# Performance work log

Hardware: AMD Instinct MI355X
Metric: run time of the kernel (lower is better)

Reference implementation:

```python
import jax, jax.numpy as jnp
import numpy as np

B, D_IN, UNITS = 4096, 1024, 1024


def setup_inputs() -> dict:
    key = jax.random.key(0)
    ks = jax.random.split(key, 8)
    scale = 1.0 / np.sqrt(D_IN + UNITS)
    return {
        "inputs": jax.random.normal(ks[0], (B, D_IN), jnp.float32),
        "hidden_state": jax.random.normal(ks[1], (B, UNITS), jnp.float32),
        "cell_state": jax.random.normal(ks[2], (B, UNITS), jnp.float32),
        "W_f": jax.random.normal(ks[3], (D_IN + UNITS, UNITS), jnp.float32) * scale,
        "b_f": jnp.ones((UNITS,), jnp.float32),  # forget gate bias initialized to ones
        "W_i": jax.random.normal(ks[4], (D_IN + UNITS, UNITS), jnp.float32) * scale,
        "b_i": jnp.zeros((UNITS,), jnp.float32),
        "W_c": jax.random.normal(ks[5], (D_IN + UNITS, UNITS), jnp.float32) * scale,
        "b_c": jnp.zeros((UNITS,), jnp.float32),
        "W_o": jax.random.normal(ks[6], (D_IN + UNITS, UNITS), jnp.float32) * scale,
        "b_o": jnp.zeros((UNITS,), jnp.float32),
    }


def reference(inputs, hidden_state, cell_state, W_f, b_f, W_i, b_i, W_c, b_c, W_o, b_o):
    # concat (hidden, inputs) along feature axis -> [B, UNITS + D_IN]
    x = jnp.concatenate((hidden_state, inputs), axis=1)
    # fuse the 4 gate projections into one GEMM: [B, 4*UNITS]
    W = jnp.concatenate((W_f, W_i, W_c, W_o), axis=1)
    b = jnp.concatenate((b_f, b_i, b_c, b_o), axis=0)
    gates = x @ W + b
    f, i, c, o = jnp.split(gates, 4, axis=1)
    forget_gate = jax.nn.sigmoid(f)
    input_gate = jax.nn.sigmoid(i)
    state_candidates = jnp.tanh(c)
    output_gate = jax.nn.sigmoid(o)
    new_cell = forget_gate * cell_state + input_gate * state_candidates
    new_hidden = output_gate * jnp.tanh(new_cell)
    return (new_hidden, new_cell)
```

## Files before the change

### kernel.cpp

```cpp
#include <hip/hip_runtime.h>

#define MDIM 4096
#define KDIM 2048
#define UDIM 1024
#define CMOFF (MDIM * UDIM)
#define NK 64
#define THREADS 512

typedef __bf16 bfrag __attribute__((ext_vector_type(8)));
typedef float f32x4 __attribute__((ext_vector_type(4)));

#define GLDS(gsrc, ldst)                                                                  \
  __builtin_amdgcn_global_load_lds((const __attribute__((address_space(1))) void*)(gsrc), \
                                   (__attribute__((address_space(3))) void*)(ldst), 16, 0, 0)

__device__ __forceinline__ unsigned short f2bf(float x) {
  unsigned int u = __float_as_uint(x);
  unsigned int r = (u + 0x7fffu + ((u >> 16) & 1u)) >> 16;
  return (unsigned short)r;
}

__device__ __forceinline__ float fast_sigmoid(float x) { return 1.f / (1.f + __expf(-x)); }

__device__ __forceinline__ float fast_tanh(float x) {
  float ax = fabsf(x);
  float e = __expf(-2.f * ax);
  float r = (1.f - e) / (1.f + e);
  return copysignf(r, x);
}

__global__ void pack_x(const float* __restrict__ hidden, const float* __restrict__ inputs,
                       unsigned short* __restrict__ A) {
  int t = blockIdx.x * blockDim.x + threadIdx.x;
  int e = t * 4;
  int m = e >> 11;
  int c = e & 2047;
  const float* src = (c < 1024) ? (hidden + m * 1024 + c) : (inputs + m * 1024 + (c - 1024));
  float4 v = *(const float4*)src;
  ushort4 o;
  o.x = f2bf(v.x);
  o.y = f2bf(v.y);
  o.z = f2bf(v.z);
  o.w = f2bf(v.w);
  *(ushort4*)(A + e) = o;
}

__global__ void pack_w(const float* __restrict__ Wf, const float* __restrict__ Wi,
                       const float* __restrict__ Wc, const float* __restrict__ Wo,
                       unsigned short* __restrict__ Wt) {
  __shared__ float tile[32][33];
  const int k0 = blockIdx.x * 32;
  const int u0 = blockIdx.y * 32;
  const int g = blockIdx.z;
  const float* W = (g == 0) ? Wf : (g == 1) ? Wi : (g == 2) ? Wc : Wo;
  const int t = threadIdx.x;
  {
    int kk = t >> 3, uu = (t & 7) * 4;
    float4 v = *(const float4*)(W + (k0 + kk) * UDIM + u0 + uu);
    tile[kk][uu + 0] = v.x;
    tile[kk][uu + 1] = v.y;
    tile[kk][uu + 2] = v.z;
    tile[kk][uu + 3] = v.w;
  }
  __syncthreads();
  {
    int ur = t >> 3, k4 = (t & 7) * 4;
    ushort4 o;
    o.x = f2bf(tile[k4 + 0][ur]);
    o.y = f2bf(tile[k4 + 1][ur]);
    o.z = f2bf(tile[k4 + 2][ur]);
    o.w = f2bf(tile[k4 + 3][ur]);
    *(ushort4*)(Wt + (size_t)(g * UDIM + u0 + ur) * KDIM + k0 + k4) = o;
  }
}

__global__ __launch_bounds__(THREADS, 2) void lstm_gemm(
    const unsigned short* __restrict__ A, const unsigned short* __restrict__ Wt,
    const float* __restrict__ bf_, const float* __restrict__ bi_,
    const float* __restrict__ bc_, const float* __restrict__ bo_,
    const float* __restrict__ cell, float* __restrict__ out) {
  extern __shared__ __bf16 lds[];

  const int tid = threadIdx.x;
  const int lane = tid & 63;
  const int wid = tid >> 6;
  const int wr = wid >> 2;
  const int wc = wid & 3;
  const int lrow = lane & 15;
  const int gb = lane >> 4;

  const int wg = blockIdx.x;
  const int swz = (wg & 7) * 32 + (wg >> 3);
  const int m0 = (swz >> 4) * 256;
  const int bn = swz & 15;

  const int G0 = tid, G1 = THREADS + tid;
  const int ar0 = G0 >> 2, ar1 = G1 >> 2;
  const unsigned short* aS0 =
      A + (size_t)(m0 + ar0) * KDIM + (((G0 & 3) ^ ((ar0 >> 1) & 3)) * 8);
  const unsigned short* aS1 =
      A + (size_t)(m0 + ar1) * KDIM + (((G1 & 3) ^ ((ar1 >> 1) & 3)) * 8);
  const int nr0 = G0 >> 2, nr1 = G1 >> 2;
  const int u_0 = bn * 64 + ((nr0 >> 6) << 4) + (nr0 & 15);
  const int u_1 = bn * 64 + ((nr1 >> 6) << 4) + (nr1 & 15);
  const int g_0 = (nr0 >> 4) & 3;
  const int g_1 = (nr1 >> 4) & 3;
  const unsigned short* bS0 =
      Wt + (size_t)(g_0 * UDIM + u_0) * KDIM + (((G0 & 3) ^ ((nr0 >> 1) & 3)) * 8);
  const unsigned short* bS1 =
      Wt + (size_t)(g_1 * UDIM + u_1) * KDIM + (((G1 & 3) ^ ((nr1 >> 1) & 3)) * 8);

  int aoff[8];
#pragma unroll
  for (int mi = 0; mi < 8; ++mi) {
    const int R = wr * 128 + mi * 16 + lrow;
    aoff[mi] = R * 32 + ((gb ^ ((R >> 1) & 3)) * 8);
  }
  int boff[4];
#pragma unroll
  for (int nf = 0; nf < 4; ++nf) {
    const int n = wc * 64 + nf * 16 + lrow;
    boff[nf] = 8192 + n * 32 + ((gb ^ ((n >> 1) & 3)) * 8);
  }

  f32x4 acc[8][4];
#pragma unroll
  for (int mi = 0; mi < 8; ++mi)
#pragma unroll
    for (int nf = 0; nf < 4; ++nf) acc[mi][nf] = (f32x4){0.f, 0.f, 0.f, 0.f};

#define STAGE_A(T, SR)                        \
  do {                                        \
    __bf16* dst_ = lds + (SR) * 16384;        \
    GLDS(aS0 + (T) * 32, dst_ + G0 * 8);      \
    GLDS(aS1 + (T) * 32, dst_ + G1 * 8);      \
  } while (0)
#define STAGE_B(T, SR)                        \
  do {                                        \
    __bf16* dst_ = lds + (SR) * 16384 + 8192; \
    GLDS(bS0 + (T) * 32, dst_ + G0 * 8);      \
    GLDS(bS1 + (T) * 32, dst_ + G1 * 8);      \
  } while (0)

  STAGE_A(0, 0);
  STAGE_B(0, 0);
  STAGE_A(1, 1);
  STAGE_B(1, 1);
  STAGE_A(2, 2);
  STAGE_B(2, 2);
  asm volatile("s_waitcnt vmcnt(8)" ::: "memory");
  __builtin_amdgcn_s_barrier();

#define TILE_BODY(T, R, SR, DO_STAGE, WAITCODE)                                        \
  do {                                                                                 \
    __bf16* ldsr_ = lds + (R) * 16384;                                                 \
    bfrag Am[4], Bm[4];                                                                \
    _Pragma("unroll") for (int mi = 0; mi < 4; ++mi) Am[mi] =                          \
        *(const bfrag*)(ldsr_ + aoff[mi]);                                             \
    _Pragma("unroll") for (int nf = 0; nf < 4; ++nf) Bm[nf] =                          \
        *(const bfrag*)(ldsr_ + boff[nf]);                                             \
    if (DO_STAGE) STAGE_A((T) + 3, SR);                                                \
    __builtin_amdgcn_s_barrier();                                                      \
    __builtin_amdgcn_s_setprio(1);                                                     \
    _Pragma("unroll") for (int mi = 0; mi < 4; ++mi)                                   \
        _Pragma("unroll") for (int nf = 0; nf < 4; ++nf) acc[mi][nf] =                 \
            __builtin_amdgcn_mfma_f32_16x16x32_bf16(Am[mi], Bm[nf], acc[mi][nf], 0, 0, 0); \
    __builtin_amdgcn_s_setprio(0);                                                     \
    bfrag A2[4];                                                                       \
    _Pragma("unroll") for (int mi = 0; mi < 4; ++mi) A2[mi] =                          \
        *(const bfrag*)(ldsr_ + aoff[4 + mi]);                                         \
    if (DO_STAGE) STAGE_B((T) + 3, SR);                                                \
    __builtin_amdgcn_s_barrier();                                                      \
    __builtin_amdgcn_s_setprio(1);                                                     \
    _Pragma("unroll") for (int mi = 0; mi < 4; ++mi)                                   \
        _Pragma("unroll") for (int nf = 0; nf < 4; ++nf) acc[4 + mi][nf] =             \
            __builtin_amdgcn_mfma_f32_16x16x32_bf16(A2[mi], Bm[nf], acc[4 + mi][nf], 0, 0, 0); \
    __builtin_amdgcn_s_setprio(0);                                                     \
    WAITCODE;                                                                          \
    __builtin_amdgcn_s_barrier();                                                      \
  } while (0)

#define VM8 asm volatile("s_waitcnt vmcnt(8)" ::: "memory")
#define VM4 asm volatile("s_waitcnt vmcnt(4)" ::: "memory")
#define VM0 asm volatile("s_waitcnt vmcnt(0)" ::: "memory")

  for (int t = 0; t < NK - 4; t += 4) {
    TILE_BODY(t + 0, 0, 3, 1, VM8);
    TILE_BODY(t + 1, 1, 0, 1, VM8);
    TILE_BODY(t + 2, 2, 1, 1, VM8);
    TILE_BODY(t + 3, 3, 2, 1, VM8);
  }
  TILE_BODY(NK - 4, 0, 3, 1, VM8);
  TILE_BODY(NK - 3, 1, 0, 0, VM4);
  TILE_BODY(NK - 2, 2, 0, 0, VM0);
  TILE_BODY(NK - 1, 3, 0, 0, );

  const int u = bn * 64 + wc * 16 + lrow;
  const float fb = bf_[u], ib = bi_[u], cb = bc_[u], ob = bo_[u];
  const int rbase = m0 + wr * 128 + (lane >> 4) * 4;
#pragma unroll
  for (int mi = 0; mi < 8; ++mi) {
#pragma unroll
    for (int j = 0; j < 4; ++j) {
      const int m = rbase + mi * 16 + j;
      float pf = acc[mi][0][j] + fb;
      float pi = acc[mi][1][j] + ib;
      float pc = acc[mi][2][j] + cb;
      float po = acc[mi][3][j] + ob;
      float fg = fast_sigmoid(pf);
      float ig = fast_sigmoid(pi);
      float cc = fast_tanh(pc);
      float og = fast_sigmoid(po);
      float cold = cell[(size_t)m * UDIM + u];
      float cnew = fg * cold + ig * cc;
      out[(size_t)m * UDIM + u] = og * fast_tanh(cnew);
      out[CMOFF + (size_t)m * UDIM + u] = cnew;
    }
  }
}

extern "C" void kernel_launch(void* const* d_in, const int* in_sizes, int n_in,
                              void* d_out, int out_size, void* d_ws, size_t ws_size,
                              hipStream_t stream) {
  const float* inputs = (const float*)d_in[0];
  const float* hidden = (const float*)d_in[1];
  const float* cell = (const float*)d_in[2];
  const float* Wf = (const float*)d_in[3];
  const float* bf = (const float*)d_in[4];
  const float* Wi = (const float*)d_in[5];
  const float* bi = (const float*)d_in[6];
  const float* Wc = (const float*)d_in[7];
  const float* bc = (const float*)d_in[8];
  const float* Wo = (const float*)d_in[9];
  const float* bo = (const float*)d_in[10];
  float* out = (float*)d_out;

  unsigned short* Abf = (unsigned short*)d_ws;
  unsigned short* Wt = Abf + (size_t)MDIM * KDIM;

  pack_x<<<(MDIM * KDIM / 4) / 256, 256, 0, stream>>>(hidden, inputs, Abf);
  pack_w<<<dim3(KDIM / 32, UDIM / 32, 4), 256, 0, stream>>>(Wf, Wi, Wc, Wo, Wt);
  lstm_gemm<<<dim3(256), dim3(THREADS), 131072, stream>>>(Abf, Wt, bf, bi, bc, bo, cell, out);
}
```

Measured before the change: 89.82 us.

## Switch GEMM to 32x32x16 MFMA with 4x2 wave layout

Replaces the 16x16x32 bf16 MFMA tiling (2x4 waves, 128x64 per wave) with 32x32x16 MFMA on a 4x2 wave grid (64x128 per wave). The B staging is permuted so each gate occupies 32-column groups, and the epilogue is remapped to the 32x32 accumulator layout. The A and B prefetches are merged into one phase with a single barrier per k-tile instead of two. The aim is fewer LDS fragment reads per MFMA and less synchronisation, at the cost of coarser overlap between loads and compute.

```diff
diff --git a/kernel.cpp b/kernel.cpp
--- a/kernel.cpp
+++ b/kernel.cpp
@@ -8,7 +8,7 @@
 #define THREADS 512
 
 typedef __bf16 bfrag __attribute__((ext_vector_type(8)));
-typedef float f32x4 __attribute__((ext_vector_type(4)));
+typedef float f32x16 __attribute__((ext_vector_type(16)));
 
 #define GLDS(gsrc, ldst)                                                                  \
   __builtin_amdgcn_global_load_lds((const __attribute__((address_space(1))) void*)(gsrc), \
@@ -84,10 +84,10 @@
   const int tid = threadIdx.x;
   const int lane = tid & 63;
   const int wid = tid >> 6;
-  const int wr = wid >> 2;
-  const int wc = wid & 3;
-  const int lrow = lane & 15;
-  const int gb = lane >> 4;
+  const int wr = wid >> 1;
+  const int wc = wid & 1;
+  const int cl = lane & 31;
+  const int hb = lane >> 5;
 
   const int wg = blockIdx.x;
   const int swz = (wg & 7) * 32 + (wg >> 3);
@@ -101,33 +101,39 @@
   const unsigned short* aS1 =
       A + (size_t)(m0 + ar1) * KDIM + (((G1 & 3) ^ ((ar1 >> 1) & 3)) * 8);
   const int nr0 = G0 >> 2, nr1 = G1 >> 2;
-  const int u_0 = bn * 64 + ((nr0 >> 6) << 4) + (nr0 & 15);
-  const int u_1 = bn * 64 + ((nr1 >> 6) << 4) + (nr1 & 15);
-  const int g_0 = (nr0 >> 4) & 3;
-  const int g_1 = (nr1 >> 4) & 3;
+  const int u_0 = bn * 64 + ((nr0 >> 7) << 5) + (nr0 & 31);
+  const int u_1 = bn * 64 + ((nr1 >> 7) << 5) + (nr1 & 31);
+  const int g_0 = (nr0 >> 5) & 3;
+  const int g_1 = (nr1 >> 5) & 3;
   const unsigned short* bS0 =
       Wt + (size_t)(g_0 * UDIM + u_0) * KDIM + (((G0 & 3) ^ ((nr0 >> 1) & 3)) * 8);
   const unsigned short* bS1 =
       Wt + (size_t)(g_1 * UDIM + u_1) * KDIM + (((G1 & 3) ^ ((nr1 >> 1) & 3)) * 8);
 
-  int aoff[8];
-#pragma unroll
-  for (int mi = 0; mi < 8; ++mi) {
-    const int R = wr * 128 + mi * 16 + lrow;
-    aoff[mi] = R * 32 + ((gb ^ ((R >> 1) & 3)) * 8);
-  }
-  int boff[4];
-#pragma unroll
-  for (int nf = 0; nf < 4; ++nf) {
-    const int n = wc * 64 + nf * 16 + lrow;
-    boff[nf] = 8192 + n * 32 + ((gb ^ ((n >> 1) & 3)) * 8);
-  }
-
-  f32x4 acc[8][4];
-#pragma unroll
-  for (int mi = 0; mi < 8; ++mi)
-#pragma unroll
-    for (int nf = 0; nf < 4; ++nf) acc[mi][nf] = (f32x4){0.f, 0.f, 0.f, 0.f};
+  int aoff2[2][2];
+#pragma unroll
+  for (int mf = 0; mf < 2; ++mf)
+#pragma unroll
+    for (int kk = 0; kk < 2; ++kk) {
+      const int R = wr * 64 + mf * 32 + cl;
+      aoff2[mf][kk] = R * 32 + (((kk * 2 + hb) ^ ((R >> 1) & 3)) * 8);
+    }
+  int boff2[4][2];
+#pragma unroll
+  for (int nf = 0; nf < 4; ++nf)
+#pragma unroll
+    for (int kk = 0; kk < 2; ++kk) {
+      const int n = wc * 128 + nf * 32 + cl;
+      boff2[nf][kk] = 8192 + n * 32 + (((kk * 2 + hb) ^ ((n >> 1) & 3)) * 8);
+    }
+
+  f32x16 acc[2][4];
+#pragma unroll
+  for (int mf = 0; mf < 2; ++mf)
+#pragma unroll
+    for (int nf = 0; nf < 4; ++nf)
+#pragma unroll
+      for (int j = 0; j < 16; ++j) acc[mf][nf][j] = 0.f;
 
 #define STAGE_A(T, SR)                        \
   do {                                        \
@@ -151,33 +157,32 @@
   asm volatile("s_waitcnt vmcnt(8)" ::: "memory");
   __builtin_amdgcn_s_barrier();
 
-#define TILE_BODY(T, R, SR, DO_STAGE, WAITCODE)                                        \
-  do {                                                                                 \
-    __bf16* ldsr_ = lds + (R) * 16384;                                                 \
-    bfrag Am[4], Bm[4];                                                                \
-    _Pragma("unroll") for (int mi = 0; mi < 4; ++mi) Am[mi] =                          \
-        *(const bfrag*)(ldsr_ + aoff[mi]);                                             \
-    _Pragma("unroll") for (int nf = 0; nf < 4; ++nf) Bm[nf] =                          \
-        *(const bfrag*)(ldsr_ + boff[nf]);                                             \
-    if (DO_STAGE) STAGE_A((T) + 3, SR);                                                \
-    __builtin_amdgcn_s_barrier();                                                      \
-    __builtin_amdgcn_s_setprio(1);                                                     \
-    _Pragma("unroll") for (int mi = 0; mi < 4; ++mi)                                   \
-        _Pragma("unroll") for (int nf = 0; nf < 4; ++nf) acc[mi][nf] =                 \
-            __builtin_amdgcn_mfma_f32_16x16x32_bf16(Am[mi], Bm[nf], acc[mi][nf], 0, 0, 0); \
-    __builtin_amdgcn_s_setprio(0);                                                     \
-    bfrag A2[4];                                                                       \
-    _Pragma("unroll") for (int mi = 0; mi < 4; ++mi) A2[mi] =                          \
-        *(const bfrag*)(ldsr_ + aoff[4 + mi]);                                         \
-    if (DO_STAGE) STAGE_B((T) + 3, SR);                                                \
-    __builtin_amdgcn_s_barrier();                                                      \
-    __builtin_amdgcn_s_setprio(1);                                                     \
-    _Pragma("unroll") for (int mi = 0; mi < 4; ++mi)                                   \
-        _Pragma("unroll") for (int nf = 0; nf < 4; ++nf) acc[4 + mi][nf] =             \
-            __builtin_amdgcn_mfma_f32_16x16x32_bf16(A2[mi], Bm[nf], acc[4 + mi][nf], 0, 0, 0); \
-    __builtin_amdgcn_s_setprio(0);                                                     \
-    WAITCODE;                                                                          \
-    __builtin_amdgcn_s_barrier();                                                      \
+#define TILE_BODY(T, R, SR, DO_STAGE, WAITCODE)                                          \
+  do {                                                                                   \
+    __bf16* ldsr_ = lds + (R) * 16384;                                                   \
+    bfrag Af[2][2], Bf[4][2];                                                            \
+    _Pragma("unroll") for (int mf = 0; mf < 2; ++mf) Af[mf][0] =                         \
+        *(const bfrag*)(ldsr_ + aoff2[mf][0]);                                           \
+    _Pragma("unroll") for (int nf = 0; nf < 4; ++nf) Bf[nf][0] =                         \
+        *(const bfrag*)(ldsr_ + boff2[nf][0]);                                           \
+    _Pragma("unroll") for (int mf = 0; mf < 2; ++mf) Af[mf][1] =                         \
+        *(const bfrag*)(ldsr_ + aoff2[mf][1]);                                           \
+    _Pragma("unroll") for (int nf = 0; nf < 4; ++nf) Bf[nf][1] =                         \
+        *(const bfrag*)(ldsr_ + boff2[nf][1]);                                           \
+    if (DO_STAGE) {                                                                      \
+      STAGE_A((T) + 3, SR);                                                              \
+      STAGE_B((T) + 3, SR);                                                              \
+    }                                                                                    \
+    __builtin_amdgcn_s_barrier();                                                        \
+    __builtin_amdgcn_s_setprio(1);                                                       \
+    _Pragma("unroll") for (int kk = 0; kk < 2; ++kk)                                     \
+        _Pragma("unroll") for (int mf = 0; mf < 2; ++mf)                                 \
+            _Pragma("unroll") for (int nf = 0; nf < 4; ++nf) acc[mf][nf] =               \
+                __builtin_amdgcn_mfma_f32_32x32x16_bf16(Af[mf][kk], Bf[nf][kk],          \
+                                                        acc[mf][nf], 0, 0, 0);           \
+    __builtin_amdgcn_s_setprio(0);                                                       \
+    WAITCODE;                                                                            \
+    __builtin_amdgcn_s_barrier();                                                        \
   } while (0)
 
 #define VM8 asm volatile("s_waitcnt vmcnt(8)" ::: "memory")
@@ -195,18 +200,18 @@
   TILE_BODY(NK - 2, 2, 0, 0, VM0);
   TILE_BODY(NK - 1, 3, 0, 0, );
 
-  const int u = bn * 64 + wc * 16 + lrow;
+  const int u = bn * 64 + wc * 32 + cl;
   const float fb = bf_[u], ib = bi_[u], cb = bc_[u], ob = bo_[u];
-  const int rbase = m0 + wr * 128 + (lane >> 4) * 4;
-#pragma unroll
-  for (int mi = 0; mi < 8; ++mi) {
-#pragma unroll
-    for (int j = 0; j < 4; ++j) {
-      const int m = rbase + mi * 16 + j;
-      float pf = acc[mi][0][j] + fb;
-      float pi = acc[mi][1][j] + ib;
-      float pc = acc[mi][2][j] + cb;
-      float po = acc[mi][3][j] + ob;
+  const int rbase = m0 + wr * 64 + 4 * hb;
+#pragma unroll
+  for (int mf = 0; mf < 2; ++mf) {
+#pragma unroll
+    for (int r = 0; r < 16; ++r) {
+      const int m = rbase + mf * 32 + (r & 3) + 8 * (r >> 2);
+      float pf = acc[mf][0][r] + fb;
+      float pi = acc[mf][1][r] + ib;
+      float pc = acc[mf][2][r] + cb;
+      float po = acc[mf][3][r] + ob;
       float fg = fast_sigmoid(pf);
       float ig = fast_sigmoid(pi);
       float cc = fast_tanh(pc);
```

New measurement: 99.18 us. 1.1x slower.

## Software-pipeline LDS fragment loads across K tiles with double-buffered registers

Applied to the files above, without the earlier changes.

Restructures the GEMM main loop so that the A/B register fragments for the next K tile are loaded from LDS during the current tile's second MFMA half, using ping-pong register sets. This hides LDS read latency behind matrix-core work and cuts one barrier per tile by merging the wait and prefetch phases. It raises register pressure from the extra fragment buffers and reorders the global-to-LDS staging relative to the barriers, which could hurt occupancy or introduce hazards if the sync ordering is subtly off.

```diff
diff --git a/kernel.cpp b/kernel.cpp
--- a/kernel.cpp
+++ b/kernel.cpp
@@ -142,58 +142,67 @@
     GLDS(bS1 + (T) * 32, dst_ + G1 * 8);      \
   } while (0)
 
+#define VM8 asm volatile("s_waitcnt vmcnt(8)" ::: "memory")
+#define VM4 asm volatile("s_waitcnt vmcnt(4)" ::: "memory")
+#define VM0 asm volatile("s_waitcnt vmcnt(0)" ::: "memory")
+
+  bfrag Fa0[4], Fb0[4], Fa1[4], Fb1[4];
+
   STAGE_A(0, 0);
   STAGE_B(0, 0);
   STAGE_A(1, 1);
   STAGE_B(1, 1);
   STAGE_A(2, 2);
   STAGE_B(2, 2);
-  asm volatile("s_waitcnt vmcnt(8)" ::: "memory");
+  VM8;
   __builtin_amdgcn_s_barrier();
-
-#define TILE_BODY(T, R, SR, DO_STAGE, WAITCODE)                                        \
-  do {                                                                                 \
-    __bf16* ldsr_ = lds + (R) * 16384;                                                 \
-    bfrag Am[4], Bm[4];                                                                \
-    _Pragma("unroll") for (int mi = 0; mi < 4; ++mi) Am[mi] =                          \
-        *(const bfrag*)(ldsr_ + aoff[mi]);                                             \
-    _Pragma("unroll") for (int nf = 0; nf < 4; ++nf) Bm[nf] =                          \
-        *(const bfrag*)(ldsr_ + boff[nf]);                                             \
-    if (DO_STAGE) STAGE_A((T) + 3, SR);                                                \
-    __builtin_amdgcn_s_barrier();                                                      \
-    __builtin_amdgcn_s_setprio(1);                                                     \
-    _Pragma("unroll") for (int mi = 0; mi < 4; ++mi)                                   \
-        _Pragma("unroll") for (int nf = 0; nf < 4; ++nf) acc[mi][nf] =                 \
-            __builtin_amdgcn_mfma_f32_16x16x32_bf16(Am[mi], Bm[nf], acc[mi][nf], 0, 0, 0); \
-    __builtin_amdgcn_s_setprio(0);                                                     \
-    bfrag A2[4];                                                                       \
-    _Pragma("unroll") for (int mi = 0; mi < 4; ++mi) A2[mi] =                          \
-        *(const bfrag*)(ldsr_ + aoff[4 + mi]);                                         \
-    if (DO_STAGE) STAGE_B((T) + 3, SR);                                                \
-    __builtin_amdgcn_s_barrier();                                                      \
-    __builtin_amdgcn_s_setprio(1);                                                     \
-    _Pragma("unroll") for (int mi = 0; mi < 4; ++mi)                                   \
-        _Pragma("unroll") for (int nf = 0; nf < 4; ++nf) acc[4 + mi][nf] =             \
-            __builtin_amdgcn_mfma_f32_16x16x32_bf16(A2[mi], Bm[nf], acc[4 + mi][nf], 0, 0, 0); \
-    __builtin_amdgcn_s_setprio(0);                                                     \
-    WAITCODE;                                                                          \
-    __builtin_amdgcn_s_barrier();                                                      \
+  __builtin_amdgcn_sched_barrier(0);
+#pragma unroll
+  for (int mi = 0; mi < 4; ++mi) Fa0[mi] = *(const bfrag*)(lds + aoff[mi]);
+#pragma unroll
+  for (int nf = 0; nf < 4; ++nf) Fb0[nf] = *(const bfrag*)(lds + boff[nf]);
+
+#define TILE_BODY(T, R, NR, SR, DO_STAGE, WAITCODE, DO_PRELOAD, CA, CB, NA, NB)          \
+  do {                                                                                   \
+    __bf16* ldsr_ = lds + (R) * 16384;                                                   \
+    __bf16* ldsn_ = lds + (NR) * 16384;                                                  \
+    if (DO_STAGE) STAGE_A((T) + 3, SR);                                                  \
+    bfrag A2[4];                                                                         \
+    _Pragma("unroll") for (int mi = 0; mi < 4; ++mi) A2[mi] =                            \
+        *(const bfrag*)(ldsr_ + aoff[4 + mi]);                                           \
+    __builtin_amdgcn_s_setprio(1);                                                       \
+    _Pragma("unroll") for (int mi = 0; mi < 4; ++mi)                                     \
+        _Pragma("unroll") for (int nf = 0; nf < 4; ++nf) acc[mi][nf] =                   \
+            __builtin_amdgcn_mfma_f32_16x16x32_bf16(CA[mi], CB[nf], acc[mi][nf], 0, 0, 0); \
+    __builtin_amdgcn_s_setprio(0);                                                       \
+    if (DO_STAGE) STAGE_B((T) + 3, SR);                                                  \
+    WAITCODE;                                                                            \
+    __builtin_amdgcn_s_barrier();                                                        \
+    __builtin_amdgcn_sched_barrier(0);                                                   \
+    if (DO_PRELOAD) {                                                                    \
+      _Pragma("unroll") for (int mi = 0; mi < 4; ++mi) NA[mi] =                          \
+          *(const bfrag*)(ldsn_ + aoff[mi]);                                             \
+      _Pragma("unroll") for (int nf = 0; nf < 4; ++nf) NB[nf] =                          \
+          *(const bfrag*)(ldsn_ + boff[nf]);                                             \
+    }                                                                                    \
+    __builtin_amdgcn_s_setprio(1);                                                       \
+    _Pragma("unroll") for (int mi = 0; mi < 4; ++mi)                                     \
+        _Pragma("unroll") for (int nf = 0; nf < 4; ++nf) acc[4 + mi][nf] =               \
+            __builtin_amdgcn_mfma_f32_16x16x32_bf16(A2[mi], CB[nf], acc[4 + mi][nf], 0, 0, 0); \
+    __builtin_amdgcn_s_setprio(0);                                                       \
+    __builtin_amdgcn_s_barrier();                                                        \
   } while (0)
 
-#define VM8 asm volatile("s_waitcnt vmcnt(8)" ::: "memory")
-#define VM4 asm volatile("s_waitcnt vmcnt(4)" ::: "memory")
-#define VM0 asm volatile("s_waitcnt vmcnt(0)" ::: "memory")
-
   for (int t = 0; t < NK - 4; t += 4) {
-    TILE_BODY(t + 0, 0, 3, 1, VM8);
-    TILE_BODY(t + 1, 1, 0, 1, VM8);
-    TILE_BODY(t + 2, 2, 1, 1, VM8);
-    TILE_BODY(t + 3, 3, 2, 1, VM8);
-  }
-  TILE_BODY(NK - 4, 0, 3, 1, VM8);
-  TILE_BODY(NK - 3, 1, 0, 0, VM4);
-  TILE_BODY(NK - 2, 2, 0, 0, VM0);
-  TILE_BODY(NK - 1, 3, 0, 0, );
+    TILE_BODY(t + 0, 0, 1, 3, 1, VM8, 1, Fa0, Fb0, Fa1, Fb1);
+    TILE_BODY(t + 1, 1, 2, 0, 1, VM8, 1, Fa1, Fb1, Fa0, Fb0);
+    TILE_BODY(t + 2, 2, 3, 1, 1, VM8, 1, Fa0, Fb0, Fa1, Fb1);
+    TILE_BODY(t + 3, 3, 0, 2, 1, VM8, 1, Fa1, Fb1, Fa0, Fb0);
+  }
+  TILE_BODY(NK - 4, 0, 1, 3, 1, VM8, 1, Fa0, Fb0, Fa1, Fb1);
+  TILE_BODY(NK - 3, 1, 2, 0, 0, VM4, 1, Fa1, Fb1, Fa0, Fb0);
+  TILE_BODY(NK - 2, 2, 3, 0, 0, VM0, 1, Fa0, Fb0, Fa1, Fb1);
+  TILE_BODY(NK - 1, 3, 0, 0, 0, ((void)0), 0, Fa1, Fb1, Fa0, Fb0);
 
   const int u = bn * 64 + wc * 16 + lrow;
   const float fb = bf_[u], ib = bi_[u], cb = bc_[u], ob = bo_[u];
```

Result: slower. 91.94 us (+2.4%).

## Double-buffer LDS fragments in registers and collapse per-tile barriers to one

Applied to the files above, without the earlier changes.

Restructures the K loop so the LDS fragments for the next tile are read with inline-asm ds_read_b128 into a second register set while the current tile's 32 MFMAs run. This cuts each tile from three barriers to one and replaces the per-fragment offset arrays with one base address plus immediate offsets. The vmcnt waits are retuned to match. It roughly doubles fragment register use and relies on hand-placed lgkmcnt waits and a sched_barrier, which risks occupancy loss or ordering hazards.

```diff
diff --git a/kernel.cpp b/kernel.cpp
--- a/kernel.cpp
+++ b/kernel.cpp
@@ -13,6 +13,9 @@
 #define GLDS(gsrc, ldst)                                                                  \
   __builtin_amdgcn_global_load_lds((const __attribute__((address_space(1))) void*)(gsrc), \
                                    (__attribute__((address_space(3))) void*)(ldst), 16, 0, 0)
+
+#define DSR(dst, addr, OFF) \
+  asm volatile("ds_read_b128 %0, %1 offset:" OFF : "=v"(dst) : "v"(addr))
 
 __device__ __forceinline__ unsigned short f2bf(float x) {
   unsigned int u = __float_as_uint(x);
@@ -110,18 +113,13 @@
   const unsigned short* bS1 =
       Wt + (size_t)(g_1 * UDIM + u_1) * KDIM + (((G1 & 3) ^ ((nr1 >> 1) & 3)) * 8);
 
-  int aoff[8];
-#pragma unroll
-  for (int mi = 0; mi < 8; ++mi) {
-    const int R = wr * 128 + mi * 16 + lrow;
-    aoff[mi] = R * 32 + ((gb ^ ((R >> 1) & 3)) * 8);
-  }
-  int boff[4];
-#pragma unroll
-  for (int nf = 0; nf < 4; ++nf) {
-    const int n = wc * 64 + nf * 16 + lrow;
-    boff[nf] = 8192 + n * 32 + ((gb ^ ((n >> 1) & 3)) * 8);
-  }
+  const int R0 = wr * 128 + lrow;
+  const int aoff0 = R0 * 32 + ((gb ^ ((R0 >> 1) & 3)) * 8);
+  const int n0 = wc * 64 + lrow;
+  const int boff0 = 8192 + n0 * 32 + ((gb ^ ((n0 >> 1) & 3)) * 8);
+  const unsigned ldsb = (unsigned)(size_t)(__attribute__((address_space(3))) void*)lds;
+  const unsigned aB = ldsb + (unsigned)aoff0 * 2u;
+  const unsigned bB = ldsb + (unsigned)boff0 * 2u;
 
   f32x4 acc[8][4];
 #pragma unroll
@@ -141,6 +139,29 @@
     GLDS(bS0 + (T) * 32, dst_ + G0 * 8);      \
     GLDS(bS1 + (T) * 32, dst_ + G1 * 8);      \
   } while (0)
+
+#define VM4 asm volatile("s_waitcnt vmcnt(4)" ::: "memory")
+#define VM0 asm volatile("s_waitcnt vmcnt(0)" ::: "memory")
+
+#define PRELOAD(PRNG, NA, NB)                      \
+  do {                                             \
+    const unsigned vA_ = aB + (PRNG)*32768u;       \
+    const unsigned vB_ = bB + (PRNG)*32768u;       \
+    DSR(NA[0], vA_, "0");                          \
+    DSR(NA[1], vA_, "1024");                       \
+    DSR(NA[2], vA_, "2048");                       \
+    DSR(NA[3], vA_, "3072");                       \
+    DSR(NA[4], vA_, "4096");                       \
+    DSR(NA[5], vA_, "5120");                       \
+    DSR(NA[6], vA_, "6144");                       \
+    DSR(NA[7], vA_, "7168");                       \
+    DSR(NB[0], vB_, "0");                          \
+    DSR(NB[1], vB_, "1024");                       \
+    DSR(NB[2], vB_, "2048");                       \
+    DSR(NB[3], vB_, "3072");                       \
+  } while (0)
+
+  bfrag Fa0[8], Fb0[4], Fa1[8], Fb1[4];
 
   STAGE_A(0, 0);
   STAGE_B(0, 0);
@@ -148,52 +169,36 @@
   STAGE_B(1, 1);
   STAGE_A(2, 2);
   STAGE_B(2, 2);
-  asm volatile("s_waitcnt vmcnt(8)" ::: "memory");
+  VM4;
   __builtin_amdgcn_s_barrier();
-
-#define TILE_BODY(T, R, SR, DO_STAGE, WAITCODE)                                        \
-  do {                                                                                 \
-    __bf16* ldsr_ = lds + (R) * 16384;                                                 \
-    bfrag Am[4], Bm[4];                                                                \
-    _Pragma("unroll") for (int mi = 0; mi < 4; ++mi) Am[mi] =                          \
-        *(const bfrag*)(ldsr_ + aoff[mi]);                                             \
-    _Pragma("unroll") for (int nf = 0; nf < 4; ++nf) Bm[nf] =                          \
-        *(const bfrag*)(ldsr_ + boff[nf]);                                             \
-    if (DO_STAGE) STAGE_A((T) + 3, SR);                                                \
-    __builtin_amdgcn_s_barrier();                                                      \
-    __builtin_amdgcn_s_setprio(1);                                                     \
-    _Pragma("unroll") for (int mi = 0; mi < 4; ++mi)                                   \
-        _Pragma("unroll") for (int nf = 0; nf < 4; ++nf) acc[mi][nf] =                 \
-            __builtin_amdgcn_mfma_f32_16x16x32_bf16(Am[mi], Bm[nf], acc[mi][nf], 0, 0, 0); \
-    __builtin_amdgcn_s_setprio(0);                                                     \
-    bfrag A2[4];                                                                       \
-    _Pragma("unroll") for (int mi = 0; mi < 4; ++mi) A2[mi] =                          \
-        *(const bfrag*)(ldsr_ + aoff[4 + mi]);                                         \
-    if (DO_STAGE) STAGE_B((T) + 3, SR);                                                \
-    __builtin_amdgcn_s_barrier();                                                      \
-    __builtin_amdgcn_s_setprio(1);                                                     \
-    _Pragma("unroll") for (int mi = 0; mi < 4; ++mi)                                   \
-        _Pragma("unroll") for (int nf = 0; nf < 4; ++nf) acc[4 + mi][nf] =             \
-            __builtin_amdgcn_mfma_f32_16x16x32_bf16(A2[mi], Bm[nf], acc[4 + mi][nf], 0, 0, 0); \
-    __builtin_amdgcn_s_setprio(0);                                                     \
-    WAITCODE;                                                                          \
-    __builtin_amdgcn_s_barrier();                                                      \
-  } while (0)
-
-#define VM8 asm volatile("s_waitcnt vmcnt(8)" ::: "memory")
-#define VM4 asm volatile("s_waitcnt vmcnt(4)" ::: "memory")
-#define VM0 asm volatile("s_waitcnt vmcnt(0)" ::: "memory")
+  PRELOAD(0, Fa0, Fb0);
+
+#define TILE_BODY(T, PRNG, SRNG, DO_STAGE, DO_PRELOAD, CA, CB, NA, NB, WAITCODE)          \
+  do {                                                                                    \
+    asm volatile("s_waitcnt lgkmcnt(0)" ::: "memory");                                    \
+    __builtin_amdgcn_sched_barrier(0);                                                    \
+    if (DO_STAGE) STAGE_A((T) + 3, SRNG);                                                 \
+    if (DO_PRELOAD) PRELOAD(PRNG, NA, NB);                                                \
+    if (DO_STAGE) STAGE_B((T) + 3, SRNG);                                                 \
+    __builtin_amdgcn_s_setprio(1);                                                        \
+    _Pragma("unroll") for (int mi = 0; mi < 8; ++mi)                                      \
+        _Pragma("unroll") for (int nf = 0; nf < 4; ++nf) acc[mi][nf] =                    \
+            __builtin_amdgcn_mfma_f32_16x16x32_bf16(CA[mi], CB[nf], acc[mi][nf], 0, 0, 0); \
+    __builtin_amdgcn_s_setprio(0);                                                        \
+    WAITCODE;                                                                             \
+    __builtin_amdgcn_s_barrier();                                                         \
+  } while (0)
 
   for (int t = 0; t < NK - 4; t += 4) {
-    TILE_BODY(t + 0, 0, 3, 1, VM8);
-    TILE_BODY(t + 1, 1, 0, 1, VM8);
-    TILE_BODY(t + 2, 2, 1, 1, VM8);
-    TILE_BODY(t + 3, 3, 2, 1, VM8);
-  }
-  TILE_BODY(NK - 4, 0, 3, 1, VM8);
-  TILE_BODY(NK - 3, 1, 0, 0, VM4);
-  TILE_BODY(NK - 2, 2, 0, 0, VM0);
-  TILE_BODY(NK - 1, 3, 0, 0, );
+    TILE_BODY(t + 0, 1, 3, 1, 1, Fa0, Fb0, Fa1, Fb1, VM4);
+    TILE_BODY(t + 1, 2, 0, 1, 1, Fa1, Fb1, Fa0, Fb0, VM4);
+    TILE_BODY(t + 2, 3, 1, 1, 1, Fa0, Fb0, Fa1, Fb1, VM4);
+    TILE_BODY(t + 3, 0, 2, 1, 1, Fa1, Fb1, Fa0, Fb0, VM4);
+  }
+  TILE_BODY(60, 1, 3, 1, 1, Fa0, Fb0, Fa1, Fb1, VM4);
+  TILE_BODY(61, 2, 0, 0, 1, Fa1, Fb1, Fa0, Fb0, VM0);
+  TILE_BODY(62, 3, 0, 0, 1, Fa0, Fb0, Fa1, Fb1, );
+  TILE_BODY(63, 0, 0, 0, 0, Fa1, Fb1, Fa0, Fb0, );
 
   const int u = bn * 64 + wc * 16 + lrow;
   const float fb = bf_[u], ib = bi_[u], cb = bc_[u], ob = bo_[u];
```

Result: slower. 137.6 us (+53.2%).
